# Kernel tuning notes

Hardware: AMD Instinct MI355X
Metric: run time of the kernel (lower is better)

## Reference

```python
import jax, jax.numpy as jnp
import numpy as np

CUTOFF = 5.0
NLINKED = 1
CELL_LIST = CUTOFF / NLINKED  # linked-cell edge length
_r = np.arange(-NLINKED, NLINKED + 1)
# torch.cartesian_prod(r1,r1,r1) == meshgrid(indexing='ij') stacked & flattened
LINKED = np.stack(np.meshgrid(_r, _r, _r, indexing='ij'), axis=-1).reshape(1, -1, 3).astype(np.float32)  # (1, 27, 3)


def setup_inputs() -> dict:
    N = 2744
    L = 30.0
    key = jax.random.key(0)
    k1, k2 = jax.random.split(key)
    coordinates = jax.random.uniform(k1, (N, 3), dtype=jnp.float32) * L
    cell = jnp.eye(3, dtype=jnp.float32) * L
    mass = jax.random.uniform(k2, (N,), dtype=jnp.float32) * 15.0 + 1.0
    period_table = jnp.ones((3,), dtype=jnp.int32)  # fully periodic
    return {"period_table": period_table, "coordinates": coordinates, "cell": cell, "mass": mass}


def _forward(period_table, coordinates, cell, mass):
    numatom = coordinates.shape[0]
    # wrap coordinates into the cell relative to atom 0 (fractional coords)
    inv_cell = jnp.linalg.inv(cell)
    inv_coor = coordinates @ inv_cell
    inv_coor = inv_coor - jnp.round(inv_coor - inv_coor[0])
    coordinates = inv_coor @ cell
    # remove center of mass
    com = (mass @ coordinates) / jnp.sum(mass)
    coordinates = coordinates - com[None, :]
    # periodic replicas needed to cover the cutoff
    num_repeats = jnp.ceil(jnp.min(CUTOFF / jnp.abs(cell), axis=0)).astype(jnp.int32)
    num_repeats = period_table.astype(jnp.int32) * num_repeats
    up = num_repeats + 1
    down = -num_repeats
    rs = [jnp.arange(int(down[i]), int(up[i])) for i in range(3)]
    g = jnp.meshgrid(*rs, indexing='ij')
    shifts_frac = jnp.stack(g, axis=-1).reshape(-1, 3).astype(coordinates.dtype)  # (S, 3)
    shifts = shifts_frac @ cell  # (S, 3) cartesian shift vectors
    num_shifts = shifts.shape[0]
    # prod = cartesian_prod(all_shifts, all_atoms).T : row0 shift idx, row1 atom idx
    prod0 = jnp.repeat(jnp.arange(num_shifts), numatom)
    prod1 = jnp.tile(jnp.arange(numatom), num_shifts)
    # shift box so all coords are positive; pad by cutoff
    mincoor = jnp.min(coordinates, axis=0) - CUTOFF - 1e-6
    coordinates = coordinates - mincoor
    maxcoor = jnp.max(coordinates, axis=0) + CUTOFF
    # all periodic images, keep only those inside the padded box
    image = (coordinates[None, :, :] + shifts[:, None, :]).reshape(-1, 3)
    keep = jnp.nonzero(((image < maxcoor) & (image > 0)).all(axis=1))[0]
    image_mask = image[keep]                      # (M, 3)
    prod0 = prod0[keep]
    prod1 = prod1[keep]
    # linked-cell indices
    ori_image_index = jnp.floor(coordinates / CELL_LIST)         # (N, 3)
    neigh_cell = ori_image_index[:, None, :] + jnp.asarray(LINKED)  # (N, 27, 3)
    image_index = jnp.floor(image_mask / CELL_LIST)              # (M, 3)
    max_cell_index = jnp.ceil(maxcoor / CELL_LIST)
    f10 = max_cell_index[1] * max_cell_index[0]
    neigh_cell_index = neigh_cell[:, :, 2] * f10 + neigh_cell[:, :, 1] * max_cell_index[0] + neigh_cell[:, :, 0]  # (N, 27)
    nimage_index = image_index[:, 2] * f10 + image_index[:, 1] * max_cell_index[0] + image_index[:, 0]            # (M,)
    # dense (N, M, 27) cell-index equality -- the memory-bound hot spot
    eq = neigh_cell_index[:, None, :] == nimage_index[None, :, None]
    ai, aj, _ = jnp.nonzero(eq)
    # distance filter on candidate pairs
    d = jnp.linalg.norm(coordinates[ai] - image_mask[aj], axis=-1)
    pair = jnp.nonzero((d < CUTOFF) & (d > 0.001))[0]
    center = ai[pair]
    img = aj[pair]
    shift_idx = prod0[img]
    atom_j = prod1[img]
    neigh_list = jnp.stack([center, atom_j])  # (2, P)
    return neigh_list, shifts[shift_idx], shifts_frac, shift_idx


def reference(period_table, coordinates, cell, mass):
    neigh_list, shifts_out, _, _ = _forward(period_table, coordinates, cell, mass)
    return (neigh_list, shifts_out)
```

## Files before the change

kernel.cpp:

```cpp
#include <hip/hip_runtime.h>
#include <math.h>

#define S_CAP   27
#define NCELLS  4096
#define MAXNB   128
#define CUT     5.0f

__global__ __launch_bounds__(256)
void k1_pre(const int* __restrict__ period, const float* __restrict__ coor,
            const float* __restrict__ cell, const float* __restrict__ mass,
            int* hdr_i, float* hdr_f, float* shifts, float* xf,
            int* __restrict__ ccount, int* __restrict__ ccur, int n)
{
    #pragma clang fp contract(off)
    __shared__ double rs[256 * 4];
    __shared__ float  redf[256 * 3];
    __shared__ float  s_com[3], s_m2[3];
    int t = threadIdx.x;

    for (int c = t; c < NCELLS; c += 256) { ccount[c] = 0; ccur[c] = 0; }

    float c[3][3];
    #pragma unroll
    for (int i = 0; i < 3; i++)
        #pragma unroll
        for (int j = 0; j < 3; j++) c[i][j] = cell[3 * i + j];

    float a00 = c[1][1]*c[2][2] - c[1][2]*c[2][1];
    float a01 = c[0][2]*c[2][1] - c[0][1]*c[2][2];
    float a02 = c[0][1]*c[1][2] - c[0][2]*c[1][1];
    float a10 = c[1][2]*c[2][0] - c[1][0]*c[2][2];
    float a11 = c[0][0]*c[2][2] - c[0][2]*c[2][0];
    float a12 = c[0][2]*c[1][0] - c[0][0]*c[1][2];
    float a20 = c[1][0]*c[2][1] - c[1][1]*c[2][0];
    float a21 = c[0][1]*c[2][0] - c[0][0]*c[2][1];
    float a22 = c[0][0]*c[1][1] - c[0][1]*c[1][0];
    float det = c[0][0]*a00 + c[0][1]*a10 + c[0][2]*a20;
    float inv[3][3] = {{a00/det, a01/det, a02/det},
                       {a10/det, a11/det, a12/det},
                       {a20/det, a21/det, a22/det}};

    float f0[3];
    #pragma unroll
    for (int d = 0; d < 3; d++)
        f0[d] = coor[0]*inv[0][d] + coor[1]*inv[1][d] + coor[2]*inv[2][d];

    double sm = 0.0, sx = 0.0, sy = 0.0, sz = 0.0;
    for (int i = t; i < n; i += 256) {
        float p0 = coor[3*i], p1 = coor[3*i+1], p2 = coor[3*i+2];
        float ic[3], w[3], x[3];
        #pragma unroll
        for (int d = 0; d < 3; d++)
            ic[d] = p0*inv[0][d] + p1*inv[1][d] + p2*inv[2][d];
        #pragma unroll
        for (int d = 0; d < 3; d++)
            w[d] = ic[d] - rintf(ic[d] - f0[d]);
        #pragma unroll
        for (int d = 0; d < 3; d++)
            x[d] = w[0]*c[0][d] + w[1]*c[1][d] + w[2]*c[2][d];
        xf[3*i] = x[0]; xf[3*i+1] = x[1]; xf[3*i+2] = x[2];
        float m = mass[i];
        sm += (double)m;
        sx += (double)m * (double)x[0];
        sy += (double)m * (double)x[1];
        sz += (double)m * (double)x[2];
    }
    rs[t] = sm; rs[256+t] = sx; rs[512+t] = sy; rs[768+t] = sz;
    __syncthreads();
    for (int off = 128; off > 0; off >>= 1) {
        if (t < off) {
            rs[t]       += rs[t+off];
            rs[256+t]   += rs[256+t+off];
            rs[512+t]   += rs[512+t+off];
            rs[768+t]   += rs[768+t+off];
        }
        __syncthreads();
    }
    if (t == 0) {
        float den = (float)rs[0];
        s_com[0] = ((float)rs[256]) / den;
        s_com[1] = ((float)rs[512]) / den;
        s_com[2] = ((float)rs[768]) / den;
    }
    __syncthreads();
    float com0 = s_com[0], com1 = s_com[1], com2 = s_com[2];

    float mn0 = __builtin_inff(), mn1 = __builtin_inff(), mn2 = __builtin_inff();
    for (int i = t; i < n; i += 256) {
        float v0 = xf[3*i]   - com0;
        float v1 = xf[3*i+1] - com1;
        float v2 = xf[3*i+2] - com2;
        xf[3*i] = v0; xf[3*i+1] = v1; xf[3*i+2] = v2;
        mn0 = fminf(mn0, v0); mn1 = fminf(mn1, v1); mn2 = fminf(mn2, v2);
    }
    redf[t] = mn0; redf[256+t] = mn1; redf[512+t] = mn2;
    __syncthreads();
    for (int off = 128; off > 0; off >>= 1) {
        if (t < off) {
            redf[t]     = fminf(redf[t],     redf[t+off]);
            redf[256+t] = fminf(redf[256+t], redf[256+t+off]);
            redf[512+t] = fminf(redf[512+t], redf[512+t+off]);
        }
        __syncthreads();
    }
    if (t == 0) {
        s_m2[0] = (redf[0]   - CUT) - 1e-6f;
        s_m2[1] = (redf[256] - CUT) - 1e-6f;
        s_m2[2] = (redf[512] - CUT) - 1e-6f;
    }
    __syncthreads();
    float m20 = s_m2[0], m21 = s_m2[1], m22 = s_m2[2];

    float mx0 = -__builtin_inff(), mx1 = -__builtin_inff(), mx2 = -__builtin_inff();
    for (int i = t; i < n; i += 256) {
        float v0 = xf[3*i]   - m20;
        float v1 = xf[3*i+1] - m21;
        float v2 = xf[3*i+2] - m22;
        xf[3*i] = v0; xf[3*i+1] = v1; xf[3*i+2] = v2;
        mx0 = fmaxf(mx0, v0); mx1 = fmaxf(mx1, v1); mx2 = fmaxf(mx2, v2);
    }
    redf[t] = mx0; redf[256+t] = mx1; redf[512+t] = mx2;
    __syncthreads();
    for (int off = 128; off > 0; off >>= 1) {
        if (t < off) {
            redf[t]     = fmaxf(redf[t],     redf[t+off]);
            redf[256+t] = fmaxf(redf[256+t], redf[256+t+off]);
            redf[512+t] = fmaxf(redf[512+t], redf[512+t+off]);
        }
        __syncthreads();
    }
    if (t == 0) {
        float maxc0 = redf[0]   + CUT;
        float maxc1 = redf[256] + CUT;
        float maxc2 = redf[512] + CUT;
        float mcell0 = ceilf(maxc0 / CUT);
        float mcell1 = ceilf(maxc1 / CUT);
        float f10 = mcell1 * mcell0;
        int nr[3];
        for (int j = 0; j < 3; j++) {
            float v = __builtin_inff();
            for (int i = 0; i < 3; i++) {
                float q = CUT / fabsf(c[i][j]);
                v = fminf(v, q);
            }
            nr[j] = (int)ceilf(v);
            nr[j] *= period[j];
        }
        int nsz0 = 2*nr[0]+1, nsz1 = 2*nr[1]+1, nsz2 = 2*nr[2]+1;
        int S = nsz0 * nsz1 * nsz2;
        if (S > S_CAP) S = S_CAP;
        hdr_i[0] = S;
        hdr_i[3] = -nr[0]; hdr_i[4] = -nr[1]; hdr_i[5] = -nr[2];
        hdr_i[6] = nsz0;   hdr_i[7] = nsz1;   hdr_i[8] = nsz2;
        hdr_i[9]  = (int)mcell0;
        hdr_i[10] = (int)f10;
        hdr_f[0] = maxc0; hdr_f[1] = maxc1; hdr_f[2] = maxc2;
        hdr_f[3] = f10;   hdr_f[4] = mcell0;
    }
    __syncthreads();
    int S = hdr_i[0];
    if (t < S) {
        int n1 = hdr_i[7], n2 = hdr_i[8];
        int i0 = t / (n1 * n2);
        int rem = t - i0 * n1 * n2;
        int i1 = rem / n2;
        int i2 = rem - i1 * n2;
        float fx = (float)(hdr_i[3] + i0);
        float fy = (float)(hdr_i[4] + i1);
        float fz = (float)(hdr_i[5] + i2);
        #pragma unroll
        for (int d = 0; d < 3; d++)
            shifts[3*t + d] = fx*c[0][d] + fy*c[1][d] + fz*c[2][d];
    }
}

__global__ __launch_bounds__(256)
void k2_count(const int* __restrict__ hdr_i, const float* __restrict__ hdr_f,
              const float* __restrict__ shifts, const float* __restrict__ xf,
              int* __restrict__ ccount, int n)
{
    #pragma clang fp contract(off)
    int g = blockIdx.x * 256 + threadIdx.x;
    int sn = hdr_i[0] * n;
    if (g >= sn) return;
    int s = g / n, a = g - s * n;
    float i0 = xf[3*a]   + shifts[3*s];
    float i1 = xf[3*a+1] + shifts[3*s+1];
    float i2 = xf[3*a+2] + shifts[3*s+2];
    bool k = (i0 > 0.0f) && (i0 < hdr_f[0]) &&
             (i1 > 0.0f) && (i1 < hdr_f[1]) &&
             (i2 > 0.0f) && (i2 < hdr_f[2]);
    if (!k) return;
    float fc0 = floorf(i0 / CUT);
    float fc1 = floorf(i1 / CUT);
    float fc2 = floorf(i2 / CUT);
    float cf = fc2 * hdr_f[3] + fc1 * hdr_f[4] + fc0;
    int ci = (int)cf;
    if (ci < 0) ci = 0;
    if (ci >= NCELLS) ci = NCELLS - 1;
    atomicAdd(&ccount[ci], 1);
}

__global__ __launch_bounds__(1024)
void k5_scan(const int* __restrict__ ccount, int* __restrict__ cstart)
{
    __shared__ int sarr[1024];
    int t = threadIdx.x;
    int b = t * 4;
    int v0 = ccount[b], v1 = ccount[b+1], v2 = ccount[b+2], v3 = ccount[b+3];
    int lsum = v0 + v1 + v2 + v3;
    sarr[t] = lsum;
    __syncthreads();
    for (int off = 1; off < 1024; off <<= 1) {
        int v = (t >= off) ? sarr[t - off] : 0;
        __syncthreads();
        sarr[t] += v;
        __syncthreads();
    }
    int excl = sarr[t] - lsum;
    cstart[b]   = excl;
    cstart[b+1] = excl + v0;
    cstart[b+2] = excl + v0 + v1;
    cstart[b+3] = excl + v0 + v1 + v2;
    if (t == 1023) cstart[NCELLS] = sarr[1023];
}

__global__ __launch_bounds__(256)
void k5b_fill(const int* __restrict__ hdr_i, const float* __restrict__ hdr_f,
              const float* __restrict__ shifts, const float* __restrict__ xf,
              const int* __restrict__ cstart, int* __restrict__ ccur,
              float4* __restrict__ bucket4, int n)
{
    #pragma clang fp contract(off)
    int g = blockIdx.x * 256 + threadIdx.x;
    int sn = hdr_i[0] * n;
    if (g >= sn) return;
    int s = g / n, a = g - s * n;
    float i0 = xf[3*a]   + shifts[3*s];
    float i1 = xf[3*a+1] + shifts[3*s+1];
    float i2 = xf[3*a+2] + shifts[3*s+2];
    bool k = (i0 > 0.0f) && (i0 < hdr_f[0]) &&
             (i1 > 0.0f) && (i1 < hdr_f[1]) &&
             (i2 > 0.0f) && (i2 < hdr_f[2]);
    if (!k) return;
    float fc0 = floorf(i0 / CUT);
    float fc1 = floorf(i1 / CUT);
    float fc2 = floorf(i2 / CUT);
    float cf = fc2 * hdr_f[3] + fc1 * hdr_f[4] + fc0;
    int ci = (int)cf;
    if (ci < 0) ci = 0;
    if (ci >= NCELLS) ci = NCELLS - 1;
    int w = cstart[ci] + atomicAdd(&ccur[ci], 1);
    bucket4[w] = make_float4(i0, i1, i2, __int_as_float(g));
}

__global__ __launch_bounds__(256)
void k6_count(const int* __restrict__ hdr_i, const float* __restrict__ xf,
              const int* __restrict__ cstart, const float4* __restrict__ bucket4,
              int* __restrict__ npair, int n)
{
    #pragma clang fp contract(off)
    int lane = threadIdx.x & 63;
    int atom = (blockIdx.x * 256 + threadIdx.x) >> 6;
    if (atom >= n) return;
    int mci = hdr_i[9], f10i = hdr_i[10];
    float x0 = xf[3*atom], x1 = xf[3*atom+1], x2 = xf[3*atom+2];
    int o0 = (int)floorf(x0 / CUT);
    int o1 = (int)floorf(x1 / CUT);
    int o2 = (int)floorf(x2 / CUT);
    int cnt = 0;
    for (int dz = -1; dz <= 1; dz++)
        for (int dy = -1; dy <= 1; dy++) {
            int nc0 = (o2+dz)*f10i + (o1+dy)*mci + (o0-1);
            int lo = nc0 < 0 ? 0 : nc0;
            int hi = nc0 + 3 > NCELLS ? NCELLS : nc0 + 3;
            if (lo >= hi) continue;
            int b0 = cstart[lo], b1 = cstart[hi];
            for (int b = b0 + lane; b < b1; b += 64) {
                float4 v = bucket4[b];
                float dxx = x0 - v.x;
                float dyy = x1 - v.y;
                float dzz = x2 - v.z;
                float ss = dxx*dxx + dyy*dyy + dzz*dzz;
                float dd = sqrtf(ss);
                if (dd < CUT && dd > 0.001f) cnt++;
            }
        }
    #pragma unroll
    for (int off = 32; off > 0; off >>= 1)
        cnt += __shfl_down(cnt, off, 64);
    if (lane == 0) npair[atom] = cnt;
}

__global__ __launch_bounds__(1024)
void k7_scan(int* hdr_i, const int* __restrict__ npair, int* __restrict__ pstart, int n)
{
    __shared__ int sarr[1024];
    int t = threadIdx.x;
    int CH = (n + 1023) >> 10;
    int base = t * CH;
    int lsum = 0;
    for (int e = 0; e < CH; e++) {
        int g = base + e;
        if (g < n) lsum += npair[g];
    }
    sarr[t] = lsum;
    __syncthreads();
    for (int off = 1; off < 1024; off <<= 1) {
        int v = (t >= off) ? sarr[t - off] : 0;
        __syncthreads();
        sarr[t] += v;
        __syncthreads();
    }
    int run = sarr[t] - lsum;
    for (int e = 0; e < CH; e++) {
        int g = base + e;
        if (g < n) { pstart[g] = run; run += npair[g]; }
    }
    if (t == 1023) pstart[n] = sarr[1023];
    if (t == 0)    hdr_i[2]  = sarr[1023];
}

__global__ __launch_bounds__(256)
void k8_emit(const int* __restrict__ hdr_i, const float* __restrict__ xf,
             const float* __restrict__ shifts, const int* __restrict__ cstart,
             const float4* __restrict__ bucket4, const int* __restrict__ pstart,
             float* __restrict__ out, int n, int P)
{
    #pragma clang fp contract(off)
    __shared__ int lst[4][MAXNB];
    int w    = threadIdx.x >> 6;
    int lane = threadIdx.x & 63;
    int atom = blockIdx.x * 4 + w;
    bool valid = atom < n;

    int mci = hdr_i[9], f10i = hdr_i[10];
    float x0 = 0.f, x1 = 0.f, x2 = 0.f;
    if (valid) { x0 = xf[3*atom]; x1 = xf[3*atom+1]; x2 = xf[3*atom+2]; }
    int o0 = (int)floorf(x0 / CUT);
    int o1 = (int)floorf(x1 / CUT);
    int o2 = (int)floorf(x2 / CUT);

    int cnt = 0;
    if (valid) {
        for (int dz = -1; dz <= 1; dz++)
            for (int dy = -1; dy <= 1; dy++) {
                int nc0 = (o2+dz)*f10i + (o1+dy)*mci + (o0-1);
                int lo = nc0 < 0 ? 0 : nc0;
                int hi = nc0 + 3 > NCELLS ? NCELLS : nc0 + 3;
                if (lo >= hi) continue;
                int b0 = cstart[lo], b1 = cstart[hi];
                for (int bb = b0; bb < b1; bb += 64) {
                    int b = bb + lane;
                    bool ok = false; int g = 0;
                    if (b < b1) {
                        float4 v = bucket4[b];
                        g = __float_as_int(v.w);
                        float dxx = x0 - v.x;
                        float dyy = x1 - v.y;
                        float dzz = x2 - v.z;
                        float ss = dxx*dxx + dyy*dyy + dzz*dzz;
                        float dd = sqrtf(ss);
                        ok = (dd < CUT) && (dd > 0.001f);
                    }
                    unsigned long long m = __ballot(ok);
                    int posn = cnt + (int)__popcll(m & ((1ull << lane) - 1ull));
                    if (ok && posn < MAXNB) lst[w][posn] = g;
                    cnt += (int)__popcll(m);
                }
            }
        if (cnt > MAXNB) cnt = MAXNB;
    }
    __syncthreads();

    if (valid) {
        int base = pstart[atom];
        for (int r = lane; r < cnt; r += 64) {
            int g = lst[w][r];
            int rank = 0;
            for (int q = 0; q < cnt; q++) rank += (lst[w][q] < g) ? 1 : 0;
            int p = base + rank;
            if (p < P) {
                int s = g / n;
                int a = g - s * n;
                out[p]     = (float)atom;
                out[P + p] = (float)a;
                out[2*P + 3*p]     = shifts[3*s];
                out[2*P + 3*p + 1] = shifts[3*s + 1];
                out[2*P + 3*p + 2] = shifts[3*s + 2];
            }
        }
    }
}

extern "C" void kernel_launch(void* const* d_in, const int* in_sizes, int n_in,
                              void* d_out, int out_size, void* d_ws, size_t ws_size,
                              hipStream_t stream)
{
    const int*   period = (const int*)d_in[0];
    const float* coor   = (const float*)d_in[1];
    const float* cell   = (const float*)d_in[2];
    const float* mass   = (const float*)d_in[3];
    float* out = (float*)d_out;

    int n  = in_sizes[1] / 3;
    int SN = S_CAP * n;
    int P  = out_size / 5;

    char* w = (char*)d_ws;
    size_t off = 0;
    auto alloc = [&](size_t bytes) -> void* {
        off = (off + 15) & ~(size_t)15;
        void* p = (void*)(w + off); off += bytes; return p;
    };

    int*    hdr_i   = (int*)   alloc(16 * 4);
    float*  hdr_f   = (float*) alloc(16 * 4);
    float*  shifts  = (float*) alloc(3 * S_CAP * 4);
    float*  xf      = (float*) alloc(3 * (size_t)n * 4);
    int*    ccount  = (int*)   alloc(NCELLS * 4);
    int*    ccur    = (int*)   alloc(NCELLS * 4);
    int*    cstart  = (int*)   alloc((NCELLS + 1) * 4);
    float4* bucket4 = (float4*)alloc((size_t)SN * 16);
    int*    npair   = (int*)   alloc((size_t)n * 4);
    int*    pstart  = (int*)   alloc(((size_t)n + 1) * 4);
    (void)ws_size; (void)n_in;

    hipMemsetAsync(d_out, 0, (size_t)out_size * 4, stream);

    int nwb = (n + 3) / 4;

    hipLaunchKernelGGL(k1_pre,   dim3(1),            dim3(256),  0, stream,
                       period, coor, cell, mass, hdr_i, hdr_f, shifts, xf, ccount, ccur, n);
    hipLaunchKernelGGL(k2_count, dim3((SN+255)/256), dim3(256),  0, stream,
                       hdr_i, hdr_f, shifts, xf, ccount, n);
    hipLaunchKernelGGL(k5_scan,  dim3(1),            dim3(1024), 0, stream,
                       ccount, cstart);
    hipLaunchKernelGGL(k5b_fill, dim3((SN+255)/256), dim3(256),  0, stream,
                       hdr_i, hdr_f, shifts, xf, cstart, ccur, bucket4, n);
    hipLaunchKernelGGL(k6_count, dim3(nwb),          dim3(256),  0, stream,
                       hdr_i, xf, cstart, bucket4, npair, n);
    hipLaunchKernelGGL(k7_scan,  dim3(1),            dim3(1024), 0, stream,
                       hdr_i, npair, pstart, n);
    hipLaunchKernelGGL(k8_emit,  dim3(nwb),          dim3(256),  0, stream,
                       hdr_i, xf, shifts, cstart, bucket4, pstart, out, n, P);
}
```

Before: 108.7 us.

## Fuse all neighbor-list stages into one cooperative persistent kernel

Replaces the memset and seven separate kernel launches with a single cooperative kernel of 256 blocks that separates the stages with grid-wide syncs. The output zeroing moves into the kernel, and the per-stage work becomes grid-stride loops. This is meant to remove launch gaps and the single-block kernel boundaries that dominate a small problem. The cost is that the serial preprocessing and the scans run on one block while every other block waits at grid.sync, and the 1024-thread scans become 256-thread scans.

```diff
diff --git a/kernel.cpp b/kernel.cpp
--- a/kernel.cpp
+++ b/kernel.cpp
@@ -1,394 +1,413 @@
 #include <hip/hip_runtime.h>
+#include <hip/hip_cooperative_groups.h>
 #include <math.h>
+
+namespace cg = cooperative_groups;
 
 #define S_CAP   27
 #define NCELLS  4096
 #define MAXNB   128
 #define CUT     5.0f
-
-__global__ __launch_bounds__(256)
-void k1_pre(const int* __restrict__ period, const float* __restrict__ coor,
-            const float* __restrict__ cell, const float* __restrict__ mass,
-            int* hdr_i, float* hdr_f, float* shifts, float* xf,
-            int* __restrict__ ccount, int* __restrict__ ccur, int n)
+#define NBLK    256
+#define NTHR    256
+
+struct Params {
+    const int*   period;
+    const float* coor;
+    const float* cell;
+    const float* mass;
+    float*       out;
+    int*         hdr_i;
+    float*       hdr_f;
+    float*       shifts;
+    float*       xf;
+    int*         ccount;
+    int*         ccur;
+    int*         cstart;
+    float4*      bucket4;
+    int*         npair;
+    int*         pstart;
+    int          n;
+    int          P;
+    int          out_size;
+};
+
+__global__ __launch_bounds__(NTHR)
+void fused(Params p)
 {
     #pragma clang fp contract(off)
-    __shared__ double rs[256 * 4];
-    __shared__ float  redf[256 * 3];
+    cg::grid_group grid = cg::this_grid();
+
+    __shared__ double rs[NTHR * 4];
+    __shared__ float  redf[NTHR * 3];
     __shared__ float  s_com[3], s_m2[3];
-    int t = threadIdx.x;
-
-    for (int c = t; c < NCELLS; c += 256) { ccount[c] = 0; ccur[c] = 0; }
-
-    float c[3][3];
-    #pragma unroll
-    for (int i = 0; i < 3; i++)
+    __shared__ int    si[NTHR];
+    __shared__ int    lst[4][MAXNB];
+
+    const int t    = threadIdx.x;
+    const int gtid = blockIdx.x * NTHR + t;
+    const int GT   = gridDim.x * NTHR;
+    const int n    = p.n;
+
+    for (int i = gtid; i < p.out_size; i += GT) p.out[i] = 0.0f;
+    for (int c = gtid; c < NCELLS; c += GT) { p.ccount[c] = 0; p.ccur[c] = 0; }
+
+    if (blockIdx.x == 0) {
+        float c[3][3];
         #pragma unroll
-        for (int j = 0; j < 3; j++) c[i][j] = cell[3 * i + j];
-
-    float a00 = c[1][1]*c[2][2] - c[1][2]*c[2][1];
-    float a01 = c[0][2]*c[2][1] - c[0][1]*c[2][2];
-    float a02 = c[0][1]*c[1][2] - c[0][2]*c[1][1];
-    float a10 = c[1][2]*c[2][0] - c[1][0]*c[2][2];
-    float a11 = c[0][0]*c[2][2] - c[0][2]*c[2][0];
-    float a12 = c[0][2]*c[1][0] - c[0][0]*c[1][2];
-    float a20 = c[1][0]*c[2][1] - c[1][1]*c[2][0];
-    float a21 = c[0][1]*c[2][0] - c[0][0]*c[2][1];
-    float a22 = c[0][0]*c[1][1] - c[0][1]*c[1][0];
-    float det = c[0][0]*a00 + c[0][1]*a10 + c[0][2]*a20;
-    float inv[3][3] = {{a00/det, a01/det, a02/det},
-                       {a10/det, a11/det, a12/det},
-                       {a20/det, a21/det, a22/det}};
-
-    float f0[3];
-    #pragma unroll
-    for (int d = 0; d < 3; d++)
-        f0[d] = coor[0]*inv[0][d] + coor[1]*inv[1][d] + coor[2]*inv[2][d];
-
-    double sm = 0.0, sx = 0.0, sy = 0.0, sz = 0.0;
-    for (int i = t; i < n; i += 256) {
-        float p0 = coor[3*i], p1 = coor[3*i+1], p2 = coor[3*i+2];
-        float ic[3], w[3], x[3];
+        for (int i = 0; i < 3; i++)
+            #pragma unroll
+            for (int j = 0; j < 3; j++) c[i][j] = p.cell[3 * i + j];
+
+        float a00 = c[1][1]*c[2][2] - c[1][2]*c[2][1];
+        float a01 = c[0][2]*c[2][1] - c[0][1]*c[2][2];
+        float a02 = c[0][1]*c[1][2] - c[0][2]*c[1][1];
+        float a10 = c[1][2]*c[2][0] - c[1][0]*c[2][2];
+        float a11 = c[0][0]*c[2][2] - c[0][2]*c[2][0];
+        float a12 = c[0][2]*c[1][0] - c[0][0]*c[1][2];
+        float a20 = c[1][0]*c[2][1] - c[1][1]*c[2][0];
+        float a21 = c[0][1]*c[2][0] - c[0][0]*c[2][1];
+        float a22 = c[0][0]*c[1][1] - c[0][1]*c[1][0];
+        float det = c[0][0]*a00 + c[0][1]*a10 + c[0][2]*a20;
+        float inv[3][3] = {{a00/det, a01/det, a02/det},
+                           {a10/det, a11/det, a12/det},
+                           {a20/det, a21/det, a22/det}};
+
+        float f0[3];
         #pragma unroll
         for (int d = 0; d < 3; d++)
-            ic[d] = p0*inv[0][d] + p1*inv[1][d] + p2*inv[2][d];
+            f0[d] = p.coor[0]*inv[0][d] + p.coor[1]*inv[1][d] + p.coor[2]*inv[2][d];
+
+        double sm = 0.0, sx = 0.0, sy = 0.0, sz = 0.0;
+        for (int i = t; i < n; i += NTHR) {
+            float p0 = p.coor[3*i], p1 = p.coor[3*i+1], p2 = p.coor[3*i+2];
+            float ic[3], w[3], x[3];
+            #pragma unroll
+            for (int d = 0; d < 3; d++)
+                ic[d] = p0*inv[0][d] + p1*inv[1][d] + p2*inv[2][d];
+            #pragma unroll
+            for (int d = 0; d < 3; d++)
+                w[d] = ic[d] - rintf(ic[d] - f0[d]);
+            #pragma unroll
+            for (int d = 0; d < 3; d++)
+                x[d] = w[0]*c[0][d] + w[1]*c[1][d] + w[2]*c[2][d];
+            p.xf[3*i] = x[0]; p.xf[3*i+1] = x[1]; p.xf[3*i+2] = x[2];
+            float m = p.mass[i];
+            sm += (double)m;
+            sx += (double)m * (double)x[0];
+            sy += (double)m * (double)x[1];
+            sz += (double)m * (double)x[2];
+        }
+        rs[t] = sm; rs[NTHR+t] = sx; rs[2*NTHR+t] = sy; rs[3*NTHR+t] = sz;
+        __syncthreads();
+        for (int off = NTHR/2; off > 0; off >>= 1) {
+            if (t < off) {
+                rs[t]          += rs[t+off];
+                rs[NTHR+t]     += rs[NTHR+t+off];
+                rs[2*NTHR+t]   += rs[2*NTHR+t+off];
+                rs[3*NTHR+t]   += rs[3*NTHR+t+off];
+            }
+            __syncthreads();
+        }
+        if (t == 0) {
+            float den = (float)rs[0];
+            s_com[0] = ((float)rs[NTHR])   / den;
+            s_com[1] = ((float)rs[2*NTHR]) / den;
+            s_com[2] = ((float)rs[3*NTHR]) / den;
+        }
+        __syncthreads();
+        float com0 = s_com[0], com1 = s_com[1], com2 = s_com[2];
+
+        float mn0 = __builtin_inff(), mn1 = __builtin_inff(), mn2 = __builtin_inff();
+        for (int i = t; i < n; i += NTHR) {
+            float v0 = p.xf[3*i]   - com0;
+            float v1 = p.xf[3*i+1] - com1;
+            float v2 = p.xf[3*i+2] - com2;
+            p.xf[3*i] = v0; p.xf[3*i+1] = v1; p.xf[3*i+2] = v2;
+            mn0 = fminf(mn0, v0); mn1 = fminf(mn1, v1); mn2 = fminf(mn2, v2);
+        }
+        redf[t] = mn0; redf[NTHR+t] = mn1; redf[2*NTHR+t] = mn2;
+        __syncthreads();
+        for (int off = NTHR/2; off > 0; off >>= 1) {
+            if (t < off) {
+                redf[t]        = fminf(redf[t],        redf[t+off]);
+                redf[NTHR+t]   = fminf(redf[NTHR+t],   redf[NTHR+t+off]);
+                redf[2*NTHR+t] = fminf(redf[2*NTHR+t], redf[2*NTHR+t+off]);
+            }
+            __syncthreads();
+        }
+        if (t == 0) {
+            s_m2[0] = (redf[0]      - CUT) - 1e-6f;
+            s_m2[1] = (redf[NTHR]   - CUT) - 1e-6f;
+            s_m2[2] = (redf[2*NTHR] - CUT) - 1e-6f;
+        }
+        __syncthreads();
+        float m20 = s_m2[0], m21 = s_m2[1], m22 = s_m2[2];
+
+        float mx0 = -__builtin_inff(), mx1 = -__builtin_inff(), mx2 = -__builtin_inff();
+        for (int i = t; i < n; i += NTHR) {
+            float v0 = p.xf[3*i]   - m20;
+            float v1 = p.xf[3*i+1] - m21;
+            float v2 = p.xf[3*i+2] - m22;
+            p.xf[3*i] = v0; p.xf[3*i+1] = v1; p.xf[3*i+2] = v2;
+            mx0 = fmaxf(mx0, v0); mx1 = fmaxf(mx1, v1); mx2 = fmaxf(mx2, v2);
+        }
+        redf[t] = mx0; redf[NTHR+t] = mx1; redf[2*NTHR+t] = mx2;
+        __syncthreads();
+        for (int off = NTHR/2; off > 0; off >>= 1) {
+            if (t < off) {
+                redf[t]        = fmaxf(redf[t],        redf[t+off]);
+                redf[NTHR+t]   = fmaxf(redf[NTHR+t],   redf[NTHR+t+off]);
+                redf[2*NTHR+t] = fmaxf(redf[2*NTHR+t], redf[2*NTHR+t+off]);
+            }
+            __syncthreads();
+        }
+        if (t == 0) {
+            float maxc0 = redf[0]      + CUT;
+            float maxc1 = redf[NTHR]   + CUT;
+            float maxc2 = redf[2*NTHR] + CUT;
+            float mcell0 = ceilf(maxc0 / CUT);
+            float mcell1 = ceilf(maxc1 / CUT);
+            float f10 = mcell1 * mcell0;
+            int nr[3];
+            for (int j = 0; j < 3; j++) {
+                float v = __builtin_inff();
+                for (int i = 0; i < 3; i++) {
+                    float q = CUT / fabsf(c[i][j]);
+                    v = fminf(v, q);
+                }
+                nr[j] = (int)ceilf(v);
+                nr[j] *= p.period[j];
+            }
+            int nsz0 = 2*nr[0]+1, nsz1 = 2*nr[1]+1, nsz2 = 2*nr[2]+1;
+            int S = nsz0 * nsz1 * nsz2;
+            if (S > S_CAP) S = S_CAP;
+            p.hdr_i[0] = S;
+            p.hdr_i[3] = -nr[0]; p.hdr_i[4] = -nr[1]; p.hdr_i[5] = -nr[2];
+            p.hdr_i[6] = nsz0;   p.hdr_i[7] = nsz1;   p.hdr_i[8] = nsz2;
+            p.hdr_i[9]  = (int)mcell0;
+            p.hdr_i[10] = (int)f10;
+            p.hdr_f[0] = maxc0; p.hdr_f[1] = maxc1; p.hdr_f[2] = maxc2;
+            p.hdr_f[3] = f10;   p.hdr_f[4] = mcell0;
+        }
+        __syncthreads();
+        int S = p.hdr_i[0];
+        if (t < S) {
+            int n1 = p.hdr_i[7], n2 = p.hdr_i[8];
+            int i0 = t / (n1 * n2);
+            int rem = t - i0 * n1 * n2;
+            int i1 = rem / n2;
+            int i2 = rem - i1 * n2;
+            float fx = (float)(p.hdr_i[3] + i0);
+            float fy = (float)(p.hdr_i[4] + i1);
+            float fz = (float)(p.hdr_i[5] + i2);
+            #pragma unroll
+            for (int d = 0; d < 3; d++)
+                p.shifts[3*t + d] = fx*c[0][d] + fy*c[1][d] + fz*c[2][d];
+        }
+    }
+    grid.sync();
+
+    {
+        int sn = p.hdr_i[0] * n;
+        float bx0 = p.hdr_f[0], bx1 = p.hdr_f[1], bx2 = p.hdr_f[2];
+        float f10 = p.hdr_f[3], mc0 = p.hdr_f[4];
+        for (int g = gtid; g < sn; g += GT) {
+            int s = g / n, a = g - s * n;
+            float i0 = p.xf[3*a]   + p.shifts[3*s];
+            float i1 = p.xf[3*a+1] + p.shifts[3*s+1];
+            float i2 = p.xf[3*a+2] + p.shifts[3*s+2];
+            bool k = (i0 > 0.0f) && (i0 < bx0) &&
+                     (i1 > 0.0f) && (i1 < bx1) &&
+                     (i2 > 0.0f) && (i2 < bx2);
+            if (!k) continue;
+            float fc0 = floorf(i0 / CUT);
+            float fc1 = floorf(i1 / CUT);
+            float fc2 = floorf(i2 / CUT);
+            float cf = fc2 * f10 + fc1 * mc0 + fc0;
+            int ci = (int)cf;
+            if (ci < 0) ci = 0;
+            if (ci >= NCELLS) ci = NCELLS - 1;
+            atomicAdd(&p.ccount[ci], 1);
+        }
+    }
+    grid.sync();
+
+    if (blockIdx.x == 0) {
+        const int CH = NCELLS / NTHR;
+        int base = t * CH;
+        int vals[NCELLS / NTHR];
+        int lsum = 0;
         #pragma unroll
-        for (int d = 0; d < 3; d++)
-            w[d] = ic[d] - rintf(ic[d] - f0[d]);
+        for (int e = 0; e < CH; e++) { vals[e] = p.ccount[base + e]; lsum += vals[e]; }
+        si[t] = lsum;
+        __syncthreads();
+        for (int off = 1; off < NTHR; off <<= 1) {
+            int v = (t >= off) ? si[t - off] : 0;
+            __syncthreads();
+            si[t] += v;
+            __syncthreads();
+        }
+        int run = si[t] - lsum;
         #pragma unroll
-        for (int d = 0; d < 3; d++)
-            x[d] = w[0]*c[0][d] + w[1]*c[1][d] + w[2]*c[2][d];
-        xf[3*i] = x[0]; xf[3*i+1] = x[1]; xf[3*i+2] = x[2];
-        float m = mass[i];
-        sm += (double)m;
-        sx += (double)m * (double)x[0];
-        sy += (double)m * (double)x[1];
-        sz += (double)m * (double)x[2];
-    }
-    rs[t] = sm; rs[256+t] = sx; rs[512+t] = sy; rs[768+t] = sz;
-    __syncthreads();
-    for (int off = 128; off > 0; off >>= 1) {
-        if (t < off) {
-            rs[t]       += rs[t+off];
-            rs[256+t]   += rs[256+t+off];
-            rs[512+t]   += rs[512+t+off];
-            rs[768+t]   += rs[768+t+off];
-        }
-        __syncthreads();
-    }
-    if (t == 0) {
-        float den = (float)rs[0];
-        s_com[0] = ((float)rs[256]) / den;
-        s_com[1] = ((float)rs[512]) / den;
-        s_com[2] = ((float)rs[768]) / den;
-    }
-    __syncthreads();
-    float com0 = s_com[0], com1 = s_com[1], com2 = s_com[2];
-
-    float mn0 = __builtin_inff(), mn1 = __builtin_inff(), mn2 = __builtin_inff();
-    for (int i = t; i < n; i += 256) {
-        float v0 = xf[3*i]   - com0;
-        float v1 = xf[3*i+1] - com1;
-        float v2 = xf[3*i+2] - com2;
-        xf[3*i] = v0; xf[3*i+1] = v1; xf[3*i+2] = v2;
-        mn0 = fminf(mn0, v0); mn1 = fminf(mn1, v1); mn2 = fminf(mn2, v2);
-    }
-    redf[t] = mn0; redf[256+t] = mn1; redf[512+t] = mn2;
-    __syncthreads();
-    for (int off = 128; off > 0; off >>= 1) {
-        if (t < off) {
-            redf[t]     = fminf(redf[t],     redf[t+off]);
-            redf[256+t] = fminf(redf[256+t], redf[256+t+off]);
-            redf[512+t] = fminf(redf[512+t], redf[512+t+off]);
-        }
-        __syncthreads();
-    }
-    if (t == 0) {
-        s_m2[0] = (redf[0]   - CUT) - 1e-6f;
-        s_m2[1] = (redf[256] - CUT) - 1e-6f;
-        s_m2[2] = (redf[512] - CUT) - 1e-6f;
-    }
-    __syncthreads();
-    float m20 = s_m2[0], m21 = s_m2[1], m22 = s_m2[2];
-
-    float mx0 = -__builtin_inff(), mx1 = -__builtin_inff(), mx2 = -__builtin_inff();
-    for (int i = t; i < n; i += 256) {
-        float v0 = xf[3*i]   - m20;
-        float v1 = xf[3*i+1] - m21;
-        float v2 = xf[3*i+2] - m22;
-        xf[3*i] = v0; xf[3*i+1] = v1; xf[3*i+2] = v2;
-        mx0 = fmaxf(mx0, v0); mx1 = fmaxf(mx1, v1); mx2 = fmaxf(mx2, v2);
-    }
-    redf[t] = mx0; redf[256+t] = mx1; redf[512+t] = mx2;
-    __syncthreads();
-    for (int off = 128; off > 0; off >>= 1) {
-        if (t < off) {
-            redf[t]     = fmaxf(redf[t],     redf[t+off]);
-            redf[256+t] = fmaxf(redf[256+t], redf[256+t+off]);
-            redf[512+t] = fmaxf(redf[512+t], redf[512+t+off]);
-        }
-        __syncthreads();
-    }
-    if (t == 0) {
-        float maxc0 = redf[0]   + CUT;
-        float maxc1 = redf[256] + CUT;
-        float maxc2 = redf[512] + CUT;
-        float mcell0 = ceilf(maxc0 / CUT);
-        float mcell1 = ceilf(maxc1 / CUT);
-        float f10 = mcell1 * mcell0;
-        int nr[3];
-        for (int j = 0; j < 3; j++) {
-            float v = __builtin_inff();
-            for (int i = 0; i < 3; i++) {
-                float q = CUT / fabsf(c[i][j]);
-                v = fminf(v, q);
-            }
-            nr[j] = (int)ceilf(v);
-            nr[j] *= period[j];
-        }
-        int nsz0 = 2*nr[0]+1, nsz1 = 2*nr[1]+1, nsz2 = 2*nr[2]+1;
-        int S = nsz0 * nsz1 * nsz2;
-        if (S > S_CAP) S = S_CAP;
-        hdr_i[0] = S;
-        hdr_i[3] = -nr[0]; hdr_i[4] = -nr[1]; hdr_i[5] = -nr[2];
-        hdr_i[6] = nsz0;   hdr_i[7] = nsz1;   hdr_i[8] = nsz2;
-        hdr_i[9]  = (int)mcell0;
-        hdr_i[10] = (int)f10;
-        hdr_f[0] = maxc0; hdr_f[1] = maxc1; hdr_f[2] = maxc2;
-        hdr_f[3] = f10;   hdr_f[4] = mcell0;
-    }
-    __syncthreads();
-    int S = hdr_i[0];
-    if (t < S) {
-        int n1 = hdr_i[7], n2 = hdr_i[8];
-        int i0 = t / (n1 * n2);
-        int rem = t - i0 * n1 * n2;
-        int i1 = rem / n2;
-        int i2 = rem - i1 * n2;
-        float fx = (float)(hdr_i[3] + i0);
-        float fy = (float)(hdr_i[4] + i1);
-        float fz = (float)(hdr_i[5] + i2);
-        #pragma unroll
-        for (int d = 0; d < 3; d++)
-            shifts[3*t + d] = fx*c[0][d] + fy*c[1][d] + fz*c[2][d];
-    }
-}
-
-__global__ __launch_bounds__(256)
-void k2_count(const int* __restrict__ hdr_i, const float* __restrict__ hdr_f,
-              const float* __restrict__ shifts, const float* __restrict__ xf,
-              int* __restrict__ ccount, int n)
-{
-    #pragma clang fp contract(off)
-    int g = blockIdx.x * 256 + threadIdx.x;
-    int sn = hdr_i[0] * n;
-    if (g >= sn) return;
-    int s = g / n, a = g - s * n;
-    float i0 = xf[3*a]   + shifts[3*s];
-    float i1 = xf[3*a+1] + shifts[3*s+1];
-    float i2 = xf[3*a+2] + shifts[3*s+2];
-    bool k = (i0 > 0.0f) && (i0 < hdr_f[0]) &&
-             (i1 > 0.0f) && (i1 < hdr_f[1]) &&
-             (i2 > 0.0f) && (i2 < hdr_f[2]);
-    if (!k) return;
-    float fc0 = floorf(i0 / CUT);
-    float fc1 = floorf(i1 / CUT);
-    float fc2 = floorf(i2 / CUT);
-    float cf = fc2 * hdr_f[3] + fc1 * hdr_f[4] + fc0;
-    int ci = (int)cf;
-    if (ci < 0) ci = 0;
-    if (ci >= NCELLS) ci = NCELLS - 1;
-    atomicAdd(&ccount[ci], 1);
-}
-
-__global__ __launch_bounds__(1024)
-void k5_scan(const int* __restrict__ ccount, int* __restrict__ cstart)
-{
-    __shared__ int sarr[1024];
-    int t = threadIdx.x;
-    int b = t * 4;
-    int v0 = ccount[b], v1 = ccount[b+1], v2 = ccount[b+2], v3 = ccount[b+3];
-    int lsum = v0 + v1 + v2 + v3;
-    sarr[t] = lsum;
-    __syncthreads();
-    for (int off = 1; off < 1024; off <<= 1) {
-        int v = (t >= off) ? sarr[t - off] : 0;
-        __syncthreads();
-        sarr[t] += v;
-        __syncthreads();
-    }
-    int excl = sarr[t] - lsum;
-    cstart[b]   = excl;
-    cstart[b+1] = excl + v0;
-    cstart[b+2] = excl + v0 + v1;
-    cstart[b+3] = excl + v0 + v1 + v2;
-    if (t == 1023) cstart[NCELLS] = sarr[1023];
-}
-
-__global__ __launch_bounds__(256)
-void k5b_fill(const int* __restrict__ hdr_i, const float* __restrict__ hdr_f,
-              const float* __restrict__ shifts, const float* __restrict__ xf,
-              const int* __restrict__ cstart, int* __restrict__ ccur,
-              float4* __restrict__ bucket4, int n)
-{
-    #pragma clang fp contract(off)
-    int g = blockIdx.x * 256 + threadIdx.x;
-    int sn = hdr_i[0] * n;
-    if (g >= sn) return;
-    int s = g / n, a = g - s * n;
-    float i0 = xf[3*a]   + shifts[3*s];
-    float i1 = xf[3*a+1] + shifts[3*s+1];
-    float i2 = xf[3*a+2] + shifts[3*s+2];
-    bool k = (i0 > 0.0f) && (i0 < hdr_f[0]) &&
-             (i1 > 0.0f) && (i1 < hdr_f[1]) &&
-             (i2 > 0.0f) && (i2 < hdr_f[2]);
-    if (!k) return;
-    float fc0 = floorf(i0 / CUT);
-    float fc1 = floorf(i1 / CUT);
-    float fc2 = floorf(i2 / CUT);
-    float cf = fc2 * hdr_f[3] + fc1 * hdr_f[4] + fc0;
-    int ci = (int)cf;
-    if (ci < 0) ci = 0;
-    if (ci >= NCELLS) ci = NCELLS - 1;
-    int w = cstart[ci] + atomicAdd(&ccur[ci], 1);
-    bucket4[w] = make_float4(i0, i1, i2, __int_as_float(g));
-}
-
-__global__ __launch_bounds__(256)
-void k6_count(const int* __restrict__ hdr_i, const float* __restrict__ xf,
-              const int* __restrict__ cstart, const float4* __restrict__ bucket4,
-              int* __restrict__ npair, int n)
-{
-    #pragma clang fp contract(off)
-    int lane = threadIdx.x & 63;
-    int atom = (blockIdx.x * 256 + threadIdx.x) >> 6;
-    if (atom >= n) return;
-    int mci = hdr_i[9], f10i = hdr_i[10];
-    float x0 = xf[3*atom], x1 = xf[3*atom+1], x2 = xf[3*atom+2];
-    int o0 = (int)floorf(x0 / CUT);
-    int o1 = (int)floorf(x1 / CUT);
-    int o2 = (int)floorf(x2 / CUT);
-    int cnt = 0;
-    for (int dz = -1; dz <= 1; dz++)
-        for (int dy = -1; dy <= 1; dy++) {
-            int nc0 = (o2+dz)*f10i + (o1+dy)*mci + (o0-1);
-            int lo = nc0 < 0 ? 0 : nc0;
-            int hi = nc0 + 3 > NCELLS ? NCELLS : nc0 + 3;
-            if (lo >= hi) continue;
-            int b0 = cstart[lo], b1 = cstart[hi];
-            for (int b = b0 + lane; b < b1; b += 64) {
-                float4 v = bucket4[b];
-                float dxx = x0 - v.x;
-                float dyy = x1 - v.y;
-                float dzz = x2 - v.z;
-                float ss = dxx*dxx + dyy*dyy + dzz*dzz;
-                float dd = sqrtf(ss);
-                if (dd < CUT && dd > 0.001f) cnt++;
-            }
-        }
-    #pragma unroll
-    for (int off = 32; off > 0; off >>= 1)
-        cnt += __shfl_down(cnt, off, 64);
-    if (lane == 0) npair[atom] = cnt;
-}
-
-__global__ __launch_bounds__(1024)
-void k7_scan(int* hdr_i, const int* __restrict__ npair, int* __restrict__ pstart, int n)
-{
-    __shared__ int sarr[1024];
-    int t = threadIdx.x;
-    int CH = (n + 1023) >> 10;
-    int base = t * CH;
-    int lsum = 0;
-    for (int e = 0; e < CH; e++) {
-        int g = base + e;
-        if (g < n) lsum += npair[g];
-    }
-    sarr[t] = lsum;
-    __syncthreads();
-    for (int off = 1; off < 1024; off <<= 1) {
-        int v = (t >= off) ? sarr[t - off] : 0;
-        __syncthreads();
-        sarr[t] += v;
-        __syncthreads();
-    }
-    int run = sarr[t] - lsum;
-    for (int e = 0; e < CH; e++) {
-        int g = base + e;
-        if (g < n) { pstart[g] = run; run += npair[g]; }
-    }
-    if (t == 1023) pstart[n] = sarr[1023];
-    if (t == 0)    hdr_i[2]  = sarr[1023];
-}
-
-__global__ __launch_bounds__(256)
-void k8_emit(const int* __restrict__ hdr_i, const float* __restrict__ xf,
-             const float* __restrict__ shifts, const int* __restrict__ cstart,
-             const float4* __restrict__ bucket4, const int* __restrict__ pstart,
-             float* __restrict__ out, int n, int P)
-{
-    #pragma clang fp contract(off)
-    __shared__ int lst[4][MAXNB];
-    int w    = threadIdx.x >> 6;
-    int lane = threadIdx.x & 63;
-    int atom = blockIdx.x * 4 + w;
-    bool valid = atom < n;
-
-    int mci = hdr_i[9], f10i = hdr_i[10];
-    float x0 = 0.f, x1 = 0.f, x2 = 0.f;
-    if (valid) { x0 = xf[3*atom]; x1 = xf[3*atom+1]; x2 = xf[3*atom+2]; }
-    int o0 = (int)floorf(x0 / CUT);
-    int o1 = (int)floorf(x1 / CUT);
-    int o2 = (int)floorf(x2 / CUT);
-
-    int cnt = 0;
-    if (valid) {
-        for (int dz = -1; dz <= 1; dz++)
-            for (int dy = -1; dy <= 1; dy++) {
-                int nc0 = (o2+dz)*f10i + (o1+dy)*mci + (o0-1);
-                int lo = nc0 < 0 ? 0 : nc0;
-                int hi = nc0 + 3 > NCELLS ? NCELLS : nc0 + 3;
-                if (lo >= hi) continue;
-                int b0 = cstart[lo], b1 = cstart[hi];
-                for (int bb = b0; bb < b1; bb += 64) {
-                    int b = bb + lane;
-                    bool ok = false; int g = 0;
-                    if (b < b1) {
-                        float4 v = bucket4[b];
-                        g = __float_as_int(v.w);
+        for (int e = 0; e < CH; e++) { p.cstart[base + e] = run; run += vals[e]; }
+        if (t == NTHR - 1) p.cstart[NCELLS] = si[NTHR - 1];
+    }
+    grid.sync();
+
+    {
+        int sn = p.hdr_i[0] * n;
+        float bx0 = p.hdr_f[0], bx1 = p.hdr_f[1], bx2 = p.hdr_f[2];
+        float f10 = p.hdr_f[3], mc0 = p.hdr_f[4];
+        for (int g = gtid; g < sn; g += GT) {
+            int s = g / n, a = g - s * n;
+            float i0 = p.xf[3*a]   + p.shifts[3*s];
+            float i1 = p.xf[3*a+1] + p.shifts[3*s+1];
+            float i2 = p.xf[3*a+2] + p.shifts[3*s+2];
+            bool k = (i0 > 0.0f) && (i0 < bx0) &&
+                     (i1 > 0.0f) && (i1 < bx1) &&
+                     (i2 > 0.0f) && (i2 < bx2);
+            if (!k) continue;
+            float fc0 = floorf(i0 / CUT);
+            float fc1 = floorf(i1 / CUT);
+            float fc2 = floorf(i2 / CUT);
+            float cf = fc2 * f10 + fc1 * mc0 + fc0;
+            int ci = (int)cf;
+            if (ci < 0) ci = 0;
+            if (ci >= NCELLS) ci = NCELLS - 1;
+            int w = p.cstart[ci] + atomicAdd(&p.ccur[ci], 1);
+            p.bucket4[w] = make_float4(i0, i1, i2, __int_as_float(g));
+        }
+    }
+    grid.sync();
+
+    {
+        int lane = t & 63;
+        int wave = gtid >> 6;
+        int NW   = GT >> 6;
+        int mci = p.hdr_i[9], f10i = p.hdr_i[10];
+        for (int atom = wave; atom < n; atom += NW) {
+            float x0 = p.xf[3*atom], x1 = p.xf[3*atom+1], x2 = p.xf[3*atom+2];
+            int o0 = (int)floorf(x0 / CUT);
+            int o1 = (int)floorf(x1 / CUT);
+            int o2 = (int)floorf(x2 / CUT);
+            int cnt = 0;
+            for (int dz = -1; dz <= 1; dz++)
+                for (int dy = -1; dy <= 1; dy++) {
+                    int nc0 = (o2+dz)*f10i + (o1+dy)*mci + (o0-1);
+                    int lo = nc0 < 0 ? 0 : nc0;
+                    int hi = nc0 + 3 > NCELLS ? NCELLS : nc0 + 3;
+                    if (lo >= hi) continue;
+                    int b0 = p.cstart[lo], b1 = p.cstart[hi];
+                    for (int b = b0 + lane; b < b1; b += 64) {
+                        float4 v = p.bucket4[b];
                         float dxx = x0 - v.x;
                         float dyy = x1 - v.y;
                         float dzz = x2 - v.z;
                         float ss = dxx*dxx + dyy*dyy + dzz*dzz;
                         float dd = sqrtf(ss);
-                        ok = (dd < CUT) && (dd > 0.001f);
+                        if (dd < CUT && dd > 0.001f) cnt++;
                     }
-                    unsigned long long m = __ballot(ok);
-                    int posn = cnt + (int)__popcll(m & ((1ull << lane) - 1ull));
-                    if (ok && posn < MAXNB) lst[w][posn] = g;
-                    cnt += (int)__popcll(m);
                 }
-            }
-        if (cnt > MAXNB) cnt = MAXNB;
-    }
-    __syncthreads();
-
-    if (valid) {
-        int base = pstart[atom];
-        for (int r = lane; r < cnt; r += 64) {
-            int g = lst[w][r];
-            int rank = 0;
-            for (int q = 0; q < cnt; q++) rank += (lst[w][q] < g) ? 1 : 0;
-            int p = base + rank;
-            if (p < P) {
-                int s = g / n;
-                int a = g - s * n;
-                out[p]     = (float)atom;
-                out[P + p] = (float)a;
-                out[2*P + 3*p]     = shifts[3*s];
-                out[2*P + 3*p + 1] = shifts[3*s + 1];
-                out[2*P + 3*p + 2] = shifts[3*s + 2];
-            }
+            #pragma unroll
+            for (int off = 32; off > 0; off >>= 1)
+                cnt += __shfl_down(cnt, off, 64);
+            if (lane == 0) p.npair[atom] = cnt;
+        }
+    }
+    grid.sync();
+
+    if (blockIdx.x == 0) {
+        int CHn = (n + NTHR - 1) / NTHR;
+        int base = t * CHn;
+        int lsum = 0;
+        for (int e = 0; e < CHn; e++) {
+            int g = base + e;
+            if (g < n) lsum += p.npair[g];
+        }
+        si[t] = lsum;
+        __syncthreads();
+        for (int off = 1; off < NTHR; off <<= 1) {
+            int v = (t >= off) ? si[t - off] : 0;
+            __syncthreads();
+            si[t] += v;
+            __syncthreads();
+        }
+        int run = si[t] - lsum;
+        for (int e = 0; e < CHn; e++) {
+            int g = base + e;
+            if (g < n) { p.pstart[g] = run; run += p.npair[g]; }
+        }
+        if (t == NTHR - 1) p.pstart[n] = si[NTHR - 1];
+    }
+    grid.sync();
+
+    {
+        int w    = t >> 6;
+        int lane = t & 63;
+        int waveg = gtid >> 6;
+        int NW    = GT >> 6;
+        int iters = (n + NW - 1) / NW;
+        int mci = p.hdr_i[9], f10i = p.hdr_i[10];
+        int P = p.P;
+        for (int it = 0; it < iters; it++) {
+            int atom = waveg + it * NW;
+            bool valid = atom < n;
+            float x0 = 0.f, x1 = 0.f, x2 = 0.f;
+            if (valid) { x0 = p.xf[3*atom]; x1 = p.xf[3*atom+1]; x2 = p.xf[3*atom+2]; }
+            int o0 = (int)floorf(x0 / CUT);
+            int o1 = (int)floorf(x1 / CUT);
+            int o2 = (int)floorf(x2 / CUT);
+            int cnt = 0;
+            if (valid) {
+                for (int dz = -1; dz <= 1; dz++)
+                    for (int dy = -1; dy <= 1; dy++) {
+                        int nc0 = (o2+dz)*f10i + (o1+dy)*mci + (o0-1);
+                        int lo = nc0 < 0 ? 0 : nc0;
+                        int hi = nc0 + 3 > NCELLS ? NCELLS : nc0 + 3;
+                        if (lo >= hi) continue;
+                        int b0 = p.cstart[lo], b1 = p.cstart[hi];
+                        for (int bb = b0; bb < b1; bb += 64) {
+                            int b = bb + lane;
+                            bool ok = false; int g = 0;
+                            if (b < b1) {
+                                float4 v = p.bucket4[b];
+                                g = __float_as_int(v.w);
+                                float dxx = x0 - v.x;
+                                float dyy = x1 - v.y;
+                                float dzz = x2 - v.z;
+                                float ss = dxx*dxx + dyy*dyy + dzz*dzz;
+                                float dd = sqrtf(ss);
+                                ok = (dd < CUT) && (dd > 0.001f);
+                            }
+                            unsigned long long m = __ballot(ok);
+                            int posn = cnt + (int)__popcll(m & ((1ull << lane) - 1ull));
+                            if (ok && posn < MAXNB) lst[w][posn] = g;
+                            cnt += (int)__popcll(m);
+                        }
+                    }
+                if (cnt > MAXNB) cnt = MAXNB;
+            }
+            __syncthreads();
+            if (valid) {
+                int base = p.pstart[atom];
+                for (int r = lane; r < cnt; r += 64) {
+                    int g = lst[w][r];
+                    int rank = 0;
+                    for (int q = 0; q < cnt; q++) rank += (lst[w][q] < g) ? 1 : 0;
+                    int pp = base + rank;
+                    if (pp < P) {
+                        int s = g / n;
+                        int a = g - s * n;
+                        p.out[pp]     = (float)atom;
+                        p.out[P + pp] = (float)a;
+                        p.out[2*P + 3*pp]     = p.shifts[3*s];
+                        p.out[2*P + 3*pp + 1] = p.shifts[3*s + 1];
+                        p.out[2*P + 3*pp + 2] = p.shifts[3*s + 2];
+                    }
+                }
+            }
+            __syncthreads();
         }
     }
 }
@@ -397,12 +416,6 @@
                               void* d_out, int out_size, void* d_ws, size_t ws_size,
                               hipStream_t stream)
 {
-    const int*   period = (const int*)d_in[0];
-    const float* coor   = (const float*)d_in[1];
-    const float* cell   = (const float*)d_in[2];
-    const float* mass   = (const float*)d_in[3];
-    float* out = (float*)d_out;
-
     int n  = in_sizes[1] / 3;
     int SN = S_CAP * n;
     int P  = out_size / 5;
@@ -411,37 +424,30 @@
     size_t off = 0;
     auto alloc = [&](size_t bytes) -> void* {
         off = (off + 15) & ~(size_t)15;
-        void* p = (void*)(w + off); off += bytes; return p;
+        void* pp = (void*)(w + off); off += bytes; return pp;
     };
 
-    int*    hdr_i   = (int*)   alloc(16 * 4);
-    float*  hdr_f   = (float*) alloc(16 * 4);
-    float*  shifts  = (float*) alloc(3 * S_CAP * 4);
-    float*  xf      = (float*) alloc(3 * (size_t)n * 4);
-    int*    ccount  = (int*)   alloc(NCELLS * 4);
-    int*    ccur    = (int*)   alloc(NCELLS * 4);
-    int*    cstart  = (int*)   alloc((NCELLS + 1) * 4);
-    float4* bucket4 = (float4*)alloc((size_t)SN * 16);
-    int*    npair   = (int*)   alloc((size_t)n * 4);
-    int*    pstart  = (int*)   alloc(((size_t)n + 1) * 4);
+    Params prm;
+    prm.period  = (const int*)d_in[0];
+    prm.coor    = (const float*)d_in[1];
+    prm.cell    = (const float*)d_in[2];
+    prm.mass    = (const float*)d_in[3];
+    prm.out     = (float*)d_out;
+    prm.hdr_i   = (int*)   alloc(16 * 4);
+    prm.hdr_f   = (float*) alloc(16 * 4);
+    prm.shifts  = (float*) alloc(3 * S_CAP * 4);
+    prm.xf      = (float*) alloc(3 * (size_t)n * 4);
+    prm.ccount  = (int*)   alloc(NCELLS * 4);
+    prm.ccur    = (int*)   alloc(NCELLS * 4);
+    prm.cstart  = (int*)   alloc((NCELLS + 1) * 4);
+    prm.bucket4 = (float4*)alloc((size_t)SN * 16);
+    prm.npair   = (int*)   alloc((size_t)n * 4);
+    prm.pstart  = (int*)   alloc(((size_t)n + 1) * 4);
+    prm.n       = n;
+    prm.P       = P;
+    prm.out_size = out_size;
     (void)ws_size; (void)n_in;
 
-    hipMemsetAsync(d_out, 0, (size_t)out_size * 4, stream);
-
-    int nwb = (n + 3) / 4;
-
-    hipLaunchKernelGGL(k1_pre,   dim3(1),            dim3(256),  0, stream,
-                       period, coor, cell, mass, hdr_i, hdr_f, shifts, xf, ccount, ccur, n);
-    hipLaunchKernelGGL(k2_count, dim3((SN+255)/256), dim3(256),  0, stream,
-                       hdr_i, hdr_f, shifts, xf, ccount, n);
-    hipLaunchKernelGGL(k5_scan,  dim3(1),            dim3(1024), 0, stream,
-                       ccount, cstart);
-    hipLaunchKernelGGL(k5b_fill, dim3((SN+255)/256), dim3(256),  0, stream,
-                       hdr_i, hdr_f, shifts, xf, cstart, ccur, bucket4, n);
-    hipLaunchKernelGGL(k6_count, dim3(nwb),          dim3(256),  0, stream,
-                       hdr_i, xf, cstart, bucket4, npair, n);
-    hipLaunchKernelGGL(k7_scan,  dim3(1),            dim3(1024), 0, stream,
-                       hdr_i, npair, pstart, n);
-    hipLaunchKernelGGL(k8_emit,  dim3(nwb),          dim3(256),  0, stream,
-                       hdr_i, xf, shifts, cstart, bucket4, pstart, out, n, P);
+    void* kp[] = { &prm };
+    hipLaunchCooperativeKernel((const void*)fused, dim3(NBLK), dim3(NTHR), kp, 0, stream);
 }
```

Measured after the change: 288.8 us. +165.7%, slower.
